# Optimization experiments

Measured on AMD Instinct MI355X. Metric: run time of the kernel, lower is better.

The kernel has to match this reference:

```python
import jax, jax.numpy as jnp
import numpy as np

D_MODEL = 1024
N_HEADS = 16
D_HEAD = D_MODEL // N_HEADS
B, S = 2, 2048


def setup_inputs() -> dict:
    key = jax.random.key(0)
    ks = jax.random.split(key, 7)
    query = jax.random.normal(ks[0], (B, S, D_MODEL), dtype=jnp.float32)
    k_in = jax.random.normal(ks[1], (B, S, D_MODEL), dtype=jnp.float32)
    v_in = jax.random.normal(ks[2], (B, S, D_MODEL), dtype=jnp.float32)
    # causal mask: True = attend allowed (torch code keeps where mask != 0)
    mask = jnp.tril(jnp.ones((S, S), dtype=bool))
    scale = 1.0 / np.sqrt(D_MODEL)
    Wq = jax.random.normal(ks[3], (D_MODEL, D_MODEL), dtype=jnp.float32) * scale
    Wk = jax.random.normal(ks[4], (D_MODEL, D_MODEL), dtype=jnp.float32) * scale
    Wv = jax.random.normal(ks[5], (D_MODEL, D_MODEL), dtype=jnp.float32) * scale
    Wo = jax.random.normal(ks[6], (D_MODEL, D_MODEL), dtype=jnp.float32) * scale
    return {"query": query, "key": k_in, "value": v_in, "mask": mask,
            "Wq": Wq, "Wk": Wk, "Wv": Wv, "Wo": Wo}


def reference(query, key, value, mask, Wq, Wk, Wv, Wo):
    b, sq, d = query.shape
    # bias-free linear: x @ W.T (torch nn.Linear convention)
    q = (query @ Wq.T).reshape(b, sq, N_HEADS, D_HEAD).transpose(0, 2, 1, 3)  # b h s d
    k = (key @ Wk.T).reshape(b, -1, N_HEADS, D_HEAD).transpose(0, 2, 1, 3)
    v = (value @ Wv.T).reshape(b, -1, N_HEADS, D_HEAD).transpose(0, 2, 1, 3)
    scores = jnp.einsum('bhqd,bhkd->bhqk', q, k) / jnp.sqrt(jnp.float32(D_HEAD))
    scores = jnp.where(mask[None, None, :, :], scores, jnp.float32(-1e9))
    attn = jax.nn.softmax(scores, axis=-1)
    # dropout is identity in eval mode
    ctx = jnp.einsum('bhqk,bhkd->bhqd', attn, v)
    ctx = ctx.transpose(0, 2, 1, 3).reshape(b, sq, d)
    return ctx @ Wo.T
```

## Files before the change

kernel.cpp:

```cpp
#include <hip/hip_runtime.h>
#include <hip/hip_bf16.h>
#include <cstdint>


typedef unsigned short u16;
typedef u16 u16x4 __attribute__((ext_vector_type(4)));
typedef u16 u16x8 __attribute__((ext_vector_type(8)));
typedef unsigned u32x2 __attribute__((ext_vector_type(2)));
typedef unsigned u32x4 __attribute__((ext_vector_type(4)));
typedef __bf16 bf16x8 __attribute__((ext_vector_type(8)));
typedef float f32x4 __attribute__((ext_vector_type(4)));

#define S_LEN 2048
#define DM 1024
#define NH 16
#define DH 64
#define BATCH 2
#define MTOT (BATCH*S_LEN)

__device__ __forceinline__ u16 f2bf(float f) {
  union { float f; unsigned u; } v; v.f = f;
  unsigned r = v.u + 0x7FFFu + ((v.u >> 16) & 1u);
  return (u16)(r >> 16);
}

__device__ __forceinline__ f32x4 mfma16(u16x8 a, u16x8 b, f32x4 c) {
  return __builtin_amdgcn_mfma_f32_16x16x32_bf16(
      __builtin_bit_cast(bf16x8, a), __builtin_bit_cast(bf16x8, b), c, 0, 0, 0);
}
__device__ __forceinline__ unsigned cvtpk_bf16(float lo, float hi) {
  unsigned r;
  asm("v_cvt_pk_bf16_f32 %0, %1, %2" : "=v"(r) : "v"(lo), "v"(hi));
  return r;
}
__device__ __forceinline__ void gload16(const u16* g, u16* l) {
  __builtin_amdgcn_global_load_lds(
      (const __attribute__((address_space(1))) unsigned int*)g,
      (__attribute__((address_space(3))) unsigned int*)l, 16, 0, 0);
}

__global__ __launch_bounds__(256) void cvt_kernel(
    const float* __restrict__ s0, const float* __restrict__ s1,
    const float* __restrict__ s2, const float* __restrict__ s3,
    u16* __restrict__ d0, u16* __restrict__ d1,
    u16* __restrict__ d2, u16* __restrict__ d3) {
  const int y = blockIdx.y;
  const float* s = (y == 0) ? s0 : (y == 1) ? s1 : (y == 2) ? s2 : s3;
  u16* d       = (y == 0) ? d0 : (y == 1) ? d1 : (y == 2) ? d2 : d3;
  int i = (blockIdx.x * 256 + threadIdx.x) * 4;
  f32x4 v = *(const f32x4*)&s[i];
  u16x4 o;
  o[0] = f2bf(v[0]); o[1] = f2bf(v[1]); o[2] = f2bf(v[2]); o[3] = f2bf(v[3]);
  *(u16x4*)&d[i] = o;
}

#define BM 128
#define BN 128
#define BKK 32

template<int MODE, bool AF32>
__device__ __forceinline__ void gemm_core(const void* __restrict__ Av,
                                          const u16* __restrict__ Bw,
                                          void* __restrict__ Cv,
                                          int K, float scale,
                                          int bx, int by, u16* smem) {
  u16* As = smem;
  u16* Bs = smem + (AF32 ? 8192 : 4096);
  float* As32 = (float*)As;
  const u16* A16 = (const u16*)Av;
  const float* A32 = (const float*)Av;
  const int tid  = threadIdx.x;
  const int lane = tid & 63, w = tid >> 6;
  const int g = lane >> 4, r16 = lane & 15;
  const int wm = w >> 1, wn = w & 1;
  const int rowBase = by * BM;
  const int colBase = bx * BN;
  f32x4 acc[4][4] = {};

  const int srowB = lane >> 2;
  const int skcB  = (lane & 3) * 8;
  const u16* gB[2]; u16* lB[2];
#pragma unroll
  for (int j = 0; j < 2; j++) {
    const int c = w * 2 + j;
    gB[j] = &Bw[(size_t)(colBase + c * 16 + srowB) * K + skcB];
    lB[j] = &Bs[c * 512];
  }
  const u16* gA16[2]; u16* lA16[2];
  const float* gA32[4]; float* lA32[4];
  if constexpr (AF32) {
    const int srow8 = lane >> 3;
    const int scF   = ((lane & 7) ^ srow8) * 4;
#pragma unroll
    for (int j = 0; j < 4; j++) {
      const int rb = w * 32 + j * 8;
      gA32[j] = &A32[(size_t)(rowBase + rb + srow8) * K + scF];
      lA32[j] = &As32[rb * 32];
    }
  } else {
#pragma unroll
    for (int j = 0; j < 2; j++) {
      const int c = w * 2 + j;
      gA16[j] = &A16[(size_t)(rowBase + c * 16 + srowB) * K + skcB];
      lA16[j] = &As[c * 512];
    }
  }

  for (int k0 = 0; k0 < K; k0 += BKK) {
    __syncthreads();
    if constexpr (AF32) {
#pragma unroll
      for (int j = 0; j < 4; j++) gload16((const u16*)(gA32[j] + k0), (u16*)lA32[j]);
    } else {
#pragma unroll
      for (int j = 0; j < 2; j++) gload16(gA16[j] + k0, lA16[j]);
    }
#pragma unroll
    for (int j = 0; j < 2; j++) gload16(gB[j] + k0, lB[j]);
    __syncthreads();
    u16x8 af[4], bfv[4];
    if constexpr (AF32) {
      const int rx = r16 & 7;
#pragma unroll
      for (int i = 0; i < 4; i++) {
        const int base = (wm * 64 + i * 16 + r16) * 32;
        f32x4 a0 = *(const f32x4*)&As32[base + (((g * 2)     ^ rx) * 4)];
        f32x4 a1 = *(const f32x4*)&As32[base + (((g * 2 + 1) ^ rx) * 4)];
        u32x4 wv = {cvtpk_bf16(a0[0], a0[1]), cvtpk_bf16(a0[2], a0[3]),
                    cvtpk_bf16(a1[0], a1[1]), cvtpk_bf16(a1[2], a1[3])};
        af[i] = __builtin_bit_cast(u16x8, wv);
      }
    } else {
#pragma unroll
      for (int i = 0; i < 4; i++)
        af[i] = *(const u16x8*)&As[(wm*64 + i*16 + r16) * BKK + g*8];
    }
#pragma unroll
    for (int j = 0; j < 4; j++) bfv[j] = *(const u16x8*)&Bs[(wn*64 + j*16 + r16) * BKK + g*8];
    __builtin_amdgcn_s_setprio(1);
#pragma unroll
    for (int i = 0; i < 4; i++)
#pragma unroll
      for (int j = 0; j < 4; j++) acc[i][j] = mfma16(af[i], bfv[j], acc[i][j]);
    __builtin_amdgcn_s_setprio(0);
  }
#pragma unroll
  for (int i = 0; i < 4; i++) {
#pragma unroll
    for (int j = 0; j < 4; j++) {
      int row = rowBase + wm*64 + i*16 + 4*g;
      int col = colBase + wn*64 + j*16 + r16;
      if (MODE == 0) {
        u16* O = (u16*)Cv;
        int head = col >> 6, d = col & 63;
#pragma unroll
        for (int r = 0; r < 4; r++)
          O[((size_t)head * MTOT + row + r) * DH + d] = f2bf(acc[i][j][r] * scale);
      } else if (MODE == 1) {
        u16x4 o;
#pragma unroll
        for (int r = 0; r < 4; r++) o[r] = f2bf(acc[i][j][r]);
        *(u16x4*)&((u16*)Cv)[(size_t)col * MTOT + row] = o;
      } else {
#pragma unroll
        for (int r = 0; r < 4; r++)
          ((float*)Cv)[(size_t)(row + r) * DM + col] = acc[i][j][r];
      }
    }
  }
}

__device__ __forceinline__ void gemm_remap(int& bx, int& by) {
  const int flat = blockIdx.x + 8 * blockIdx.y;
  const int xcd = flat & 7, i = flat >> 3;
  bx = i & 7;
  by = xcd * 4 + (i >> 3);
}

__global__ __launch_bounds__(256) void qkv_proj_kernel(
    const float* __restrict__ Xq, const float* __restrict__ Xk, const float* __restrict__ Xv,
    const u16* __restrict__ Wq, const u16* __restrict__ Wk, const u16* __restrict__ Wv,
    u16* __restrict__ Qp, u16* __restrict__ Kp, u16* __restrict__ Vt) {
  __shared__ u16 smem[12288];
  int bx, by; gemm_remap(bx, by);
  const int z = blockIdx.z;
  if (z == 0)      gemm_core<0, true>(Xq, Wq, Qp, DM, 0.125f * 1.44269504f, bx, by, smem);
  else if (z == 1) gemm_core<0, true>(Xk, Wk, Kp, DM, 1.0f, bx, by, smem);
  else             gemm_core<1, true>(Xv, Wv, Vt, DM, 1.0f, bx, by, smem);
}

__global__ __launch_bounds__(256) void out_proj_kernel(
    const u16* __restrict__ Ctx, const u16* __restrict__ Wo, float* __restrict__ Out) {
  __shared__ u16 smem[8192];
  int bx, by; gemm_remap(bx, by);
  gemm_core<2, false>(Ctx, Wo, Out, DM, 1.0f, bx, by, smem);
}


#define STAGE(B, T)                                                            \
  {                                                                            \
    const int kv0_ = (T) * 64;                                                 \
    _Pragma("unroll")                                                          \
    for (int j = 0; j < 2; j++) {                                              \
      const int rb = wv * 16 + j * 8;                                          \
      gload16(&Kbase[(size_t)(kv0_ + rb + srow) * DH + sc16 * 8],              \
              &Kl[B][rb * 64]);                                                \
      gload16(&Vbase[(size_t)(rb + srow) * MTOT + kv0_ + sc16 * 8],            \
              &Vl[B][rb * 64]);                                                \
    }                                                                          \
  }

#define TILE_BODY(BUF, T)                                                      \
  {                                                                            \
    const int kv0 = (T) * 64;                                                  \
    f32x4 s[4] = {};                                                           \
    __builtin_amdgcn_s_setprio(1);                                             \
    _Pragma("unroll")                                                          \
    for (int f = 0; f < 4; f++) {                                              \
      _Pragma("unroll")                                                        \
      for (int ds = 0; ds < 2; ds++) {                                         \
        u16x8 kf = *(const u16x8*)&Kl[BUF][(f * 16 + q16) * 64 +               \
                                           ((ds * 4 + g) ^ qx7) * 8];          \
        s[f] = mfma16(kf, qf[ds], s[f]);                                       \
      }                                                                        \
    }                                                                          \
    __builtin_amdgcn_s_setprio(0);                                             \
    if ((T) == ntb - 1) {             \
      const int qg = qb16 + q16;                                               \
      _Pragma("unroll")                                                        \
      for (int f = 0; f < 4; f++)                                              \
        _Pragma("unroll")                                                      \
        for (int r = 0; r < 4; r++)                                            \
          if (kv0 + f * 16 + 4 * g + r > qg) s[f][r] = -1e30f;                 \
    }                                                                          \
    float mx[4];                                                               \
    _Pragma("unroll")                                                          \
    for (int r = 0; r < 4; r++)                                                \
      mx[r] = fmaxf(fmaxf(s[0][r], s[1][r]), fmaxf(s[2][r], s[3][r]));         \
    float pmax = fmaxf(fmaxf(mx[0], mx[1]), fmaxf(mx[2], mx[3]));              \
    pmax = fmaxf(pmax, __shfl_xor(pmax, 16, 64));                              \
    pmax = fmaxf(pmax, __shfl_xor(pmax, 32, 64));                              \
    if (__ballot(pmax > m + 11.5f)) {              \
      float mnew = fmaxf(m, pmax);                                             \
      float alpha = exp2f(m - mnew);                                           \
      l *= alpha; m = mnew;                                                    \
      float fsc[4];                                                            \
      _Pragma("unroll")                                                        \
      for (int r = 0; r < 4; r++) fsc[r] = __shfl(alpha, 4 * g + r, 64);       \
      _Pragma("unroll")                                                        \
      for (int dt = 0; dt < 4; dt++)                                           \
        _Pragma("unroll")                                                      \
        for (int r = 0; r < 4; r++) ctx[dt][r] *= fsc[r];                      \
    }                                                                          \
    _Pragma("unroll")                                                          \
    for (int f = 0; f < 4; f++)                                                \
      _Pragma("unroll")                                                        \
      for (int r = 0; r < 4; r++) s[f][r] = exp2f(s[f][r] - m);                \
    f32x4 sv = (s[0] + s[1]) + (s[2] + s[3]);                                  \
    float psum = (sv[0] + sv[1]) + (sv[2] + sv[3]);                            \
    psum += __shfl_xor(psum, 16, 64);                                          \
    psum += __shfl_xor(psum, 32, 64);                                          \
    l += psum;                                                                 \
            \
    _Pragma("unroll")                                                          \
    for (int f = 0; f < 4; f++) {                                              \
      const int cidx = (((2 * f + (g >> 1)) ^ qx7) * 8) + 4 * (g & 1);         \
      u32x2 pw = {cvtpk_bf16(s[f][0], s[f][1]), cvtpk_bf16(s[f][2], s[f][3])}; \
      *(u32x2*)&P16[q16 * 64 + cidx] = pw;                                     \
    }                                                                          \
    asm volatile("s_waitcnt lgkmcnt(0)" ::: "memory");                         \
    __builtin_amdgcn_sched_barrier(0);                                         \
    u16x8 pa0 = *(const u16x8*)&P16[q16 * 64 + ((g)     ^ qx7) * 8];           \
    u16x8 pa1 = *(const u16x8*)&P16[q16 * 64 + ((4 + g) ^ qx7) * 8];           \
    __builtin_amdgcn_s_setprio(1);                                             \
    _Pragma("unroll")                                                          \
    for (int dt = 0; dt < 4; dt++) {                                           \
      u16x8 vf0 = *(const u16x8*)&Vl[BUF][(dt * 16 + q16) * 64 +               \
                                          ((g)     ^ qx7) * 8];                \
      u16x8 vf1 = *(const u16x8*)&Vl[BUF][(dt * 16 + q16) * 64 +               \
                                          ((4 + g) ^ qx7) * 8];                \
      ctx[dt] = mfma16(pa0, vf0, ctx[dt]);                                     \
      ctx[dt] = mfma16(pa1, vf1, ctx[dt]);                                     \
    }                                                                          \
    __builtin_amdgcn_s_setprio(0);                                             \
  }

__global__ __launch_bounds__(256, 4) void attn_kernel(const u16* __restrict__ Qp,
                                                      const u16* __restrict__ Kp,
                                                      const u16* __restrict__ Vt,
                                                      u16* __restrict__ Ctx) {
  __shared__ u16 Kl[2][64 * 64];
  __shared__ u16 Vl[2][64 * 64];
  __shared__ u16 Pl[4][16 * 64];
  const int tid = threadIdx.x;
  const int lane = tid & 63, wv = tid >> 6;
  const int q16 = lane & 15, g = lane >> 4;
  const int qx7 = q16 & 7;
  const int flat = blockIdx.x;
  const int xcd = flat & 7, idx = flat >> 3;
  const int bh = xcd * 4 + (idx & 3);
  const int qc = 31 - (idx >> 2);
  const int bb = bh >> 4, h = bh & 15;
  const int qb16 = qc * 64 + wv * 16;

  const u16* Qbase = Qp + (size_t)(h * MTOT + bb * S_LEN) * DH;
  const u16* Kbase = Kp + (size_t)(h * MTOT + bb * S_LEN) * DH;
  const u16* Vbase = Vt + (size_t)(h * DH) * MTOT + bb * S_LEN;
  u16* P16 = Pl[wv];

  u16x8 qf[2];
#pragma unroll
  for (int ds = 0; ds < 2; ds++)
    qf[ds] = *(const u16x8*)&Qbase[(size_t)(qb16 + q16) * DH + ds * 32 + g * 8];

  f32x4 ctx[4] = {};
  float m = -3.0e38f, l = 0.f;
  const int ntb = qc + 1;

  const int srow = lane >> 3;
  const int sc16 = (lane & 7) ^ srow;

  STAGE(0, 0);
  int cur = 0;
  for (int t = 0; t < ntb; ++t) {
    __syncthreads();
    if (t + 1 < ntb) STAGE(cur ^ 1, t + 1);
    TILE_BODY(cur, t);
    cur ^= 1;
  }

  const float linv = 1.f / l;
  float flv[4];
#pragma unroll
  for (int r = 0; r < 4; r++) flv[r] = __shfl(linv, 4 * g + r, 64);
#pragma unroll
  for (int dt = 0; dt < 4; dt++)
#pragma unroll
    for (int r = 0; r < 4; r++) {
      size_t grow = (size_t)(bb * S_LEN + qb16 + 4 * g + r) * DM + h * DH;
      Ctx[grow + dt * 16 + q16] = f2bf(ctx[dt][r] * flv[r]);
    }
}

extern "C" void kernel_launch(void* const* d_in, const int* in_sizes, int n_in,
                              void* d_out, int out_size, void* d_ws, size_t ws_size,
                              hipStream_t stream) {
  const float* q_in = (const float*)d_in[0];
  const float* k_in = (const float*)d_in[1];
  const float* v_in = (const float*)d_in[2];
  const float* wq = (const float*)d_in[4];
  const float* wk = (const float*)d_in[5];
  const float* wv = (const float*)d_in[6];
  const float* wo = (const float*)d_in[7];

  char* ws = (char*)d_ws;
  const size_t MB = 1024ull * 1024ull;
  u16* Qp  = (u16*)(ws + 0  * MB);
  u16* Kp  = (u16*)(ws + 8  * MB);
  u16* Vt  = (u16*)(ws + 16 * MB);
  u16* Ctx = (u16*)(ws + 24 * MB);
  u16* Wqb = (u16*)(ws + 56 * MB);
  u16* Wkb = (u16*)(ws + 58 * MB);
  u16* Wvb = (u16*)(ws + 60 * MB);
  u16* Wob = (u16*)(ws + 62 * MB);

  cvt_kernel<<<dim3(DM * DM / 1024, 4), 256, 0, stream>>>(
      wq, wk, wv, wo, Wqb, Wkb, Wvb, Wob);
  qkv_proj_kernel<<<dim3(DM / BN, MTOT / BM, 3), 256, 0, stream>>>(
      q_in, k_in, v_in, Wqb, Wkb, Wvb, Qp, Kp, Vt);
  attn_kernel<<<dim3(1024), 256, 0, stream>>>(Qp, Kp, Vt, Ctx);
  out_proj_kernel<<<dim3(DM / BN, MTOT / BM), 256, 0, stream>>>(Ctx, Wob, (float*)d_out);
}
```

Before: 122.3 us.

## Double-buffer GEMM shared-memory tiles to overlap global loads with MFMA

The projection GEMM core now uses two LDS buffers and prefetches the next K-tile while running MFMAs on the current one. This drops one of the two barriers per iteration and is meant to hide global load latency behind compute. LDS use per block doubles (48KB for QKV, 32KB for the output projection), which may reduce occupancy. The barrier logic depends on gload16 being waited on before the next __syncthreads, and no explicit vmcnt wait is added.

```diff
diff --git a/kernel.cpp b/kernel.cpp
--- a/kernel.cpp
+++ b/kernel.cpp
@@ -64,9 +64,8 @@
                                           void* __restrict__ Cv,
                                           int K, float scale,
                                           int bx, int by, u16* smem) {
-  u16* As = smem;
-  u16* Bs = smem + (AF32 ? 8192 : 4096);
-  float* As32 = (float*)As;
+  const int BUFSZ = AF32 ? 12288 : 8192;
+  const int AOFF  = AF32 ? 8192  : 4096;
   const u16* A16 = (const u16*)Av;
   const float* A32 = (const float*)Av;
   const int tid  = threadIdx.x;
@@ -79,15 +78,15 @@
 
   const int srowB = lane >> 2;
   const int skcB  = (lane & 3) * 8;
-  const u16* gB[2]; u16* lB[2];
+  const u16* gB[2]; int oB[2];
 #pragma unroll
   for (int j = 0; j < 2; j++) {
     const int c = w * 2 + j;
     gB[j] = &Bw[(size_t)(colBase + c * 16 + srowB) * K + skcB];
-    lB[j] = &Bs[c * 512];
-  }
-  const u16* gA16[2]; u16* lA16[2];
-  const float* gA32[4]; float* lA32[4];
+    oB[j] = c * 512;
+  }
+  const u16* gA16[2]; int oA16[2];
+  const float* gA32[4]; int oA32[4];
   if constexpr (AF32) {
     const int srow8 = lane >> 3;
     const int scF   = ((lane & 7) ^ srow8) * 4;
@@ -95,37 +94,59 @@
     for (int j = 0; j < 4; j++) {
       const int rb = w * 32 + j * 8;
       gA32[j] = &A32[(size_t)(rowBase + rb + srow8) * K + scF];
-      lA32[j] = &As32[rb * 32];
+      oA32[j] = rb * 32;
     }
   } else {
 #pragma unroll
     for (int j = 0; j < 2; j++) {
       const int c = w * 2 + j;
       gA16[j] = &A16[(size_t)(rowBase + c * 16 + srowB) * K + skcB];
-      lA16[j] = &As[c * 512];
-    }
-  }
-
-  for (int k0 = 0; k0 < K; k0 += BKK) {
+      oA16[j] = c * 512;
+    }
+  }
+
+  const int NT = K / BKK;
+  {
+    u16* base = smem;
+    if constexpr (AF32) {
+      float* a32 = (float*)base;
+#pragma unroll
+      for (int j = 0; j < 4; j++) gload16((const u16*)gA32[j], (u16*)(a32 + oA32[j]));
+    } else {
+#pragma unroll
+      for (int j = 0; j < 2; j++) gload16(gA16[j], base + oA16[j]);
+    }
+#pragma unroll
+    for (int j = 0; j < 2; j++) gload16(gB[j], base + AOFF + oB[j]);
+  }
+  int cur = 0;
+  for (int t = 0; t < NT; ++t) {
     __syncthreads();
-    if constexpr (AF32) {
-#pragma unroll
-      for (int j = 0; j < 4; j++) gload16((const u16*)(gA32[j] + k0), (u16*)lA32[j]);
-    } else {
-#pragma unroll
-      for (int j = 0; j < 2; j++) gload16(gA16[j] + k0, lA16[j]);
-    }
-#pragma unroll
-    for (int j = 0; j < 2; j++) gload16(gB[j] + k0, lB[j]);
-    __syncthreads();
+    if (t + 1 < NT) {
+      const int k0 = (t + 1) * BKK;
+      u16* base = smem + (cur ^ 1) * BUFSZ;
+      if constexpr (AF32) {
+        float* a32 = (float*)base;
+#pragma unroll
+        for (int j = 0; j < 4; j++) gload16((const u16*)(gA32[j] + k0), (u16*)(a32 + oA32[j]));
+      } else {
+#pragma unroll
+        for (int j = 0; j < 2; j++) gload16(gA16[j] + k0, base + oA16[j]);
+      }
+#pragma unroll
+      for (int j = 0; j < 2; j++) gload16(gB[j] + k0, base + AOFF + oB[j]);
+    }
+    u16* As = smem + cur * BUFSZ;
+    u16* Bs = As + AOFF;
+    float* As32 = (float*)As;
     u16x8 af[4], bfv[4];
     if constexpr (AF32) {
       const int rx = r16 & 7;
 #pragma unroll
       for (int i = 0; i < 4; i++) {
-        const int base = (wm * 64 + i * 16 + r16) * 32;
-        f32x4 a0 = *(const f32x4*)&As32[base + (((g * 2)     ^ rx) * 4)];
-        f32x4 a1 = *(const f32x4*)&As32[base + (((g * 2 + 1) ^ rx) * 4)];
+        const int base_ = (wm * 64 + i * 16 + r16) * 32;
+        f32x4 a0 = *(const f32x4*)&As32[base_ + (((g * 2)     ^ rx) * 4)];
+        f32x4 a1 = *(const f32x4*)&As32[base_ + (((g * 2 + 1) ^ rx) * 4)];
         u32x4 wv = {cvtpk_bf16(a0[0], a0[1]), cvtpk_bf16(a0[2], a0[3]),
                     cvtpk_bf16(a1[0], a1[1]), cvtpk_bf16(a1[2], a1[3])};
         af[i] = __builtin_bit_cast(u16x8, wv);
@@ -143,6 +164,7 @@
 #pragma unroll
       for (int j = 0; j < 4; j++) acc[i][j] = mfma16(af[i], bfv[j], acc[i][j]);
     __builtin_amdgcn_s_setprio(0);
+    cur ^= 1;
   }
 #pragma unroll
   for (int i = 0; i < 4; i++) {
@@ -181,7 +203,7 @@
     const float* __restrict__ Xq, const float* __restrict__ Xk, const float* __restrict__ Xv,
     const u16* __restrict__ Wq, const u16* __restrict__ Wk, const u16* __restrict__ Wv,
     u16* __restrict__ Qp, u16* __restrict__ Kp, u16* __restrict__ Vt) {
-  __shared__ u16 smem[12288];
+  __shared__ u16 smem[24576];
   int bx, by; gemm_remap(bx, by);
   const int z = blockIdx.z;
   if (z == 0)      gemm_core<0, true>(Xq, Wq, Qp, DM, 0.125f * 1.44269504f, bx, by, smem);
@@ -191,7 +213,7 @@
 
 __global__ __launch_bounds__(256) void out_proj_kernel(
     const u16* __restrict__ Ctx, const u16* __restrict__ Wo, float* __restrict__ Out) {
-  __shared__ u16 smem[8192];
+  __shared__ u16 smem[16384];
   int bx, by; gemm_remap(bx, by);
   gemm_core<2, false>(Ctx, Wo, Out, DM, 1.0f, bx, by, smem);
 }
@@ -366,8 +388,8 @@
 
   cvt_kernel<<<dim3(DM * DM / 1024, 4), 256, 0, stream>>>(
       wq, wk, wv, wo, Wqb, Wkb, Wvb, Wob);
-  qkv_proj_kernel<<<dim3(DM / BN, MTOT / BM, 3), 256, 0, stream>>>(
+  qkv_proj_kernel<<<dim3(8, MTOT / BM, 3), 256, 0, stream>>>(
       q_in, k_in, v_in, Wqb, Wkb, Wvb, Qp, Kp, Vt);
   attn_kernel<<<dim3(1024), 256, 0, stream>>>(Qp, Kp, Vt, Ctx);
-  out_proj_kernel<<<dim3(DM / BN, MTOT / BM), 256, 0, stream>>>(Ctx, Wob, (float*)d_out);
-}
+  out_proj_kernel<<<dim3(8, MTOT / BM), 256, 0, stream>>>(Ctx, Wob, (float*)d_out);
+}
```

Measured after the change: 117.0 us. 1.05x faster.
